# Optimization experiments

Hardware: AMD Instinct MI355X
Metric: run time of the kernel (lower is better)

The kernel has to match this reference:

```python
import jax, jax.numpy as jnp
import numpy as np
import math

HEAD_DIM = 128
N_HEADS = 32
N_KV_HEADS = 8
HIDDEN = 4096
ROPE_BASE = 10000.0


def _rope_cos_sin(position_ids):
    # inv_freq: [D/2]
    inv_freq = 1.0 / (ROPE_BASE ** (jnp.arange(0, HEAD_DIM, 2, dtype=jnp.float32) / HEAD_DIM))
    freqs = position_ids.astype(jnp.float32)[..., None] * inv_freq  # [B,S,D/2]
    emb = jnp.concatenate([freqs, freqs], axis=-1)  # [B,S,D]
    return jnp.cos(emb), jnp.sin(emb)


def _rotate_half(x):
    x1, x2 = jnp.split(x, 2, axis=-1)
    return jnp.concatenate([-x2, x1], axis=-1)


def setup_inputs() -> dict:
    key = jax.random.key(0)
    ks = jax.random.split(key, 5)
    B, S = 1, 2048
    inp = {
        "hidden_states": jax.random.normal(ks[0], (B, S, HIDDEN), dtype=jnp.float32),
        "position_ids": jnp.arange(B * S, dtype=jnp.int32).reshape(B, S),
        "Wq": jax.random.normal(ks[1], (HIDDEN, N_HEADS * HEAD_DIM), dtype=jnp.float32) * 0.02,
        "Wk": jax.random.normal(ks[2], (HIDDEN, N_KV_HEADS * HEAD_DIM), dtype=jnp.float32) * 0.02,
        "Wv": jax.random.normal(ks[3], (HIDDEN, N_KV_HEADS * HEAD_DIM), dtype=jnp.float32) * 0.02,
        "Wo": jax.random.normal(ks[4], (N_HEADS * HEAD_DIM, HIDDEN), dtype=jnp.float32) * 0.02,
    }
    return inp


def reference(hidden_states, position_ids, Wq, Wk, Wv, Wo):
    B, S, _ = hidden_states.shape
    G = N_HEADS // N_KV_HEADS

    q = (hidden_states @ Wq).reshape(B, S, N_HEADS, HEAD_DIM).transpose(0, 2, 1, 3)      # [B,H,S,D]
    k = (hidden_states @ Wk).reshape(B, S, N_KV_HEADS, HEAD_DIM).transpose(0, 2, 1, 3)   # [B,Hkv,S,D]
    v = (hidden_states @ Wv).reshape(B, S, N_KV_HEADS, HEAD_DIM).transpose(0, 2, 1, 3)

    cos, sin = _rope_cos_sin(position_ids)          # [B,S,D]
    cos = cos[:, None, :, :]                         # [B,1,S,D]
    sin = sin[:, None, :, :]
    q = q * cos + _rotate_half(q) * sin
    k = k * cos + _rotate_half(k) * sin

    # GQA head expansion (repeat_interleave over head dim)
    k = jnp.repeat(k, G, axis=1)                     # [B,H,S,D]
    v = jnp.repeat(v, G, axis=1)

    scale = 1.0 / math.sqrt(HEAD_DIM)
    scores = jnp.einsum("bhqd,bhkd->bhqk", q, k) * scale  # [B,H,S,S]
    causal = jnp.triu(jnp.full((S, S), -jnp.inf, dtype=scores.dtype), k=1)
    scores = scores + causal[None, None]
    probs = jax.nn.softmax(scores.astype(jnp.float32), axis=-1).astype(q.dtype)
    ctx = jnp.einsum("bhqk,bhkd->bhqd", probs, v)    # [B,H,S,D]
    ctx = ctx.transpose(0, 2, 1, 3).reshape(B, S, N_HEADS * HEAD_DIM)
    return ctx @ Wo
```

## Files before the change

kernel.cpp:

```cpp
#include <hip/hip_runtime.h>
#include <hip/hip_bf16.h>
#include <math.h>

#define SEQ 2048
#define NHEADS 32
#define NKVH 8
#define HD 128
#define HIDDEN 4096
#define NQKV 6144

typedef unsigned short u16;
typedef unsigned int u32;
typedef __attribute__((ext_vector_type(8))) __bf16 bf16x8;
typedef __attribute__((ext_vector_type(4))) float f32x4;
typedef __attribute__((ext_vector_type(4))) u16 u16x4;
typedef __attribute__((ext_vector_type(4))) u32 u32x4;

__device__ __forceinline__ u16 f2bf(float f) {
  u32 u = __builtin_bit_cast(u32, f);
  u32 r = (u + 0x7fffu + ((u >> 16) & 1u)) >> 16;
  return (u16)r;
}
__device__ __forceinline__ float bf2f(u16 h) {
  return __builtin_bit_cast(float, ((u32)h) << 16);
}
__device__ __forceinline__ void gload_lds16(const void* g, void* l) {
  __builtin_amdgcn_global_load_lds(
      (const __attribute__((address_space(1))) u32*)g,
      (__attribute__((address_space(3))) u32*)l, 16, 0, 0);
}

#define BAR __builtin_amdgcn_s_barrier()
#define PRIO1 __builtin_amdgcn_s_setprio(1)
#define PRIO0 __builtin_amdgcn_s_setprio(0)
#define VMW(n) asm volatile("s_waitcnt vmcnt(" #n ")" ::: "memory")

__global__ void __launch_bounds__(256) prep_all(
    const float* __restrict__ hs, u16* __restrict__ Xb,
    const float* __restrict__ Wq, u16* __restrict__ Wqt,
    const float* __restrict__ Wk, u16* __restrict__ Wkt,
    const float* __restrict__ Wv, u16* __restrict__ Wvt) {
  const int bid = blockIdx.x;
  if (bid < 8192) {
    const int i = (bid * 256 + threadIdx.x) * 4;
    const float4 v = *(const float4*)(hs + i);
    u16x4 o;
    o.x = f2bf(v.x); o.y = f2bf(v.y); o.z = f2bf(v.z); o.w = f2bf(v.w);
    *(u16x4*)(Xb + i) = o;
    return;
  }
  __shared__ float tile[64][65];
  const float* src; u16* dst; int C, lc, tb;
  const int b2 = bid - 8192;
  if (b2 < 4096) { src = Wq; dst = Wqt; C = 4096; lc = 6; tb = b2; }
  else if (b2 < 5120) { src = Wk; dst = Wkt; C = 1024; lc = 4; tb = b2 - 4096; }
  else { src = Wv; dst = Wvt; C = 1024; lc = 4; tb = b2 - 5120; }
  const int r0 = (tb >> lc) * 64, c0 = (tb & ((1 << lc) - 1)) * 64;
  const int tx = threadIdx.x & 63, ty = threadIdx.x >> 6;
#pragma unroll
  for (int j = 0; j < 16; ++j)
    tile[ty + j * 4][tx] = src[(size_t)(r0 + ty + j * 4) * C + c0 + tx];
  __syncthreads();
#pragma unroll
  for (int j = 0; j < 16; ++j)
    dst[(size_t)(c0 + ty + j * 4) * 4096 + r0 + tx] = f2bf(tile[tx][ty + j * 4]);
}

__global__ void __launch_bounds__(256) post_qkv(u16* __restrict__ qkv, u16* __restrict__ vtb,
                                                const int* __restrict__ pos,
                                                const float* __restrict__ Wsrc,
                                                u16* __restrict__ Wdst) {
  const int bid = blockIdx.x;
  if (bid < 20480) {
    int idx, hoff, sshift;
    float oscale;
    if (bid < 16384) {
      idx = bid * 256 + threadIdx.x;
      hoff = ((idx >> 6) & 31) * 128;
      sshift = 11;
      oscale = 0.08838834764831845f * 1.44269504088896340f;
    } else {
      idx = (bid - 16384) * 256 + threadIdx.x;
      hoff = 4096 + ((idx >> 6) & 7) * 128;
      sshift = 9;
      oscale = 1.0f;
    }
    const int j = idx & 63;
    const int s = idx >> sshift;
    if (s >= SEQ) return;
    const float p = (float)pos[s];
    const float invf = __expf((float)j * -0.14391156831212787f);
    const float ang = p * invf;
    const float c = cosf(ang), sn = sinf(ang);
    u16* bp = qkv + (size_t)s * NQKV + hoff + j;
    const float x1 = bf2f(bp[0]), x2 = bf2f(bp[64]);
    bp[0] = f2bf((x1 * c - x2 * sn) * oscale);
    bp[64] = f2bf((x2 * c + x1 * sn) * oscale);
    return;
  }
  if (bid < 22528) {
    __shared__ u16 tile[32][34];
    const int b2 = bid - 20480;
    const int c0 = (b2 & 31) * 32, r0 = (b2 >> 5) * 32;
    const int tx = threadIdx.x & 31, ty = threadIdx.x >> 5;
#pragma unroll
    for (int i = 0; i < 4; ++i)
      tile[ty + i * 8][tx] = qkv[(size_t)(r0 + ty + i * 8) * NQKV + 5120 + c0 + tx];
    __syncthreads();
#pragma unroll
    for (int i = 0; i < 4; ++i)
      vtb[(size_t)(c0 + ty + i * 8) * 2048 + r0 + tx] = tile[tx][ty + i * 8];
    return;
  }
  __shared__ float tf[64][65];
  const int tb = bid - 22528;
  const int r0 = (tb >> 6) * 64, c0 = (tb & 63) * 64;
  const int tx = threadIdx.x & 63, ty = threadIdx.x >> 6;
#pragma unroll
  for (int j = 0; j < 16; ++j)
    tf[ty + j * 4][tx] = Wsrc[(size_t)(r0 + ty + j * 4) * 4096 + c0 + tx];
  __syncthreads();
#pragma unroll
  for (int j = 0; j < 16; ++j)
    Wdst[(size_t)(c0 + ty + j * 4) * 4096 + r0 + tx] = f2bf(tf[tx][ty + j * 4]);
}

__global__ void __launch_bounds__(512) gemm_qkv(
    const u16* __restrict__ A, const u16* __restrict__ B, u16* __restrict__ C) {
  __shared__ u16 As[2][256 * 64];
  __shared__ u16 Bs[2][192 * 64];
  const int t = threadIdx.x;
  const int lane = t & 63, w = t >> 6;
  const int wr = w >> 2, wc = w & 3;
  const int l15 = lane & 15, l4 = lane >> 4;

  const int bid = blockIdx.x;
  const int xcd = bid & 7, ii = bid >> 3;
  const int byt = xcd, bxt = ii;
  const int row0 = byt * 256, col0 = bxt * 192;

  auto stageA_part = [&](int buf, int tile, int gfirst) {
#pragma unroll
    for (int gg = 0; gg < 2; ++gg) {
      const int g = gfirst + gg * 2;
      const int o = (g * 512 + t) * 16;
      const int ridx = o >> 7;
      const int slot = (o >> 4) & 7;
      gload_lds16(A + (size_t)(row0 + ridx) * 4096 + (tile << 6) + ((slot ^ (ridx & 7)) << 3),
                  (char*)&As[buf][0] + o);
    }
  };
  auto stageB = [&](int buf, int tile) {
#pragma unroll
    for (int g = 0; g < 3; ++g) {
      const int o = (g * 512 + t) * 16;
      const int ridx = o >> 7;
      const int slot = (o >> 4) & 7;
      gload_lds16(B + (size_t)(col0 + ridx) * 4096 + (tile << 6) + ((slot ^ (ridx & 7)) << 3),
                  (char*)&Bs[buf][0] + o);
    }
  };

  bf16x8 af[4][2], bfr[3][2];
  auto loadA = [&](int buf, int mh) {
#pragma unroll
    for (int f = 0; f < 4; ++f)
#pragma unroll
      for (int ks = 0; ks < 2; ++ks) {
        const int idx2 = wr * 128 + mh * 64 + f * 16 + l15;
        const int slot = ks * 4 + l4;
        af[f][ks] = *(const bf16x8*)((const char*)&As[buf][0] + idx2 * 128 +
                                     ((slot ^ (idx2 & 7)) << 4));
      }
  };
  auto loadB = [&](int buf) {
#pragma unroll
    for (int e = 0; e < 3; ++e)
#pragma unroll
      for (int ks = 0; ks < 2; ++ks) {
        const int idx2 = wc * 48 + e * 16 + l15;
        const int slot = ks * 4 + l4;
        bfr[e][ks] = *(const bf16x8*)((const char*)&Bs[buf][0] + idx2 * 128 +
                                      ((slot ^ (idx2 & 7)) << 4));
      }
  };

  f32x4 acc0[4][3], acc1[4][3];
#pragma unroll
  for (int f = 0; f < 4; ++f)
#pragma unroll
    for (int e = 0; e < 3; ++e) {
      acc0[f][e] = f32x4{0.f, 0.f, 0.f, 0.f};
      acc1[f][e] = f32x4{0.f, 0.f, 0.f, 0.f};
    }

  const int nkt = 4096 >> 6;

  stageA_part(0, 0, 0); stageA_part(0, 0, 1); stageB(0, 0);
  stageA_part(1, 1, 0); stageA_part(1, 1, 1); stageB(1, 1);
  VMW(7);
  BAR;

  for (int kt = 0; kt < nkt; ++kt) {
    const int buf = kt & 1;
    loadA(buf, 0); loadB(buf);
    if (kt >= 1 && kt + 1 < nkt) { stageA_part(buf ^ 1, kt + 1, 1); stageB(buf ^ 1, kt + 1); }
    BAR;
    PRIO1;
#pragma unroll
    for (int f = 0; f < 4; ++f)
#pragma unroll
      for (int e = 0; e < 3; ++e)
#pragma unroll
        for (int ks = 0; ks < 2; ++ks)
          acc0[f][e] = __builtin_amdgcn_mfma_f32_16x16x32_bf16(af[f][ks], bfr[e][ks], acc0[f][e],
                                                               0, 0, 0);
    PRIO0;
    BAR;
    loadA(buf, 1);
    if (kt + 2 < nkt) stageA_part(buf, kt + 2, 0);
    BAR;
    PRIO1;
#pragma unroll
    for (int f = 0; f < 4; ++f)
#pragma unroll
      for (int e = 0; e < 3; ++e)
#pragma unroll
        for (int ks = 0; ks < 2; ++ks)
          acc1[f][e] = __builtin_amdgcn_mfma_f32_16x16x32_bf16(af[f][ks], bfr[e][ks], acc1[f][e],
                                                               0, 0, 0);
    PRIO0;
    if (kt + 2 < nkt) { VMW(2); } else { VMW(0); }
    BAR;
  }

#pragma unroll
  for (int f = 0; f < 4; ++f)
#pragma unroll
    for (int e = 0; e < 3; ++e) {
      const int colb = col0 + wc * 48 + e * 16 + l15;
      const int r0a = row0 + wr * 128 + f * 16 + l4 * 4;
#pragma unroll
      for (int r = 0; r < 4; ++r)
        C[(size_t)(r0a + r) * NQKV + colb] = f2bf(acc0[f][e][r]);
      const int r0b = r0a + 64;
#pragma unroll
      for (int r = 0; r < 4; ++r)
        C[(size_t)(r0b + r) * NQKV + colb] = f2bf(acc1[f][e][r]);
    }
}

template <int MH, int NH>
__device__ __forceinline__ void mfq16(f32x4 (&acc)[4][4], const bf16x8 (&af)[2][2],
                                      const bf16x8 (&b)[2][2]) {
#pragma unroll
  for (int f = 0; f < 2; ++f)
#pragma unroll
    for (int e = 0; e < 2; ++e)
#pragma unroll
      for (int ks = 0; ks < 2; ++ks)
        acc[MH * 2 + f][NH * 2 + e] = __builtin_amdgcn_mfma_f32_16x16x32_bf16(
            af[f][ks], b[e][ks], acc[MH * 2 + f][NH * 2 + e], 0, 0, 0);
}

__global__ void __launch_bounds__(512, 2) gemm8p16(
    const u16* __restrict__ A, const u16* __restrict__ B, float* __restrict__ C) {
  __shared__ u16 As[2][2][64 * 64];
  __shared__ u16 Bs[2][2][128 * 64];
  const int t = threadIdx.x;
  const int lane = t & 63, w = t >> 6;
  const int wr = w >> 2, wc = w & 3;
  const int l15 = lane & 15, l4 = lane >> 4;

  const int flat = blockIdx.x;
  const int xcd = flat & 7, idx = flat >> 3;
  const int bxt = idx & 15, byt = xcd * 2 + (idx >> 4);
  const int row0 = byt * 128, col0 = bxt * 256;

  auto stageA = [&](int buf, int half, int tile) {
    const int o = t * 16;
    const int ridx = o >> 7;
    const int slot = (o >> 4) & 7;
    const int gr = (ridx >> 5) * 64 + half * 32 + (ridx & 31);
    gload_lds16(A + (size_t)(row0 + gr) * 4096 + (tile << 6) + ((slot ^ (ridx & 7)) << 3),
                (char*)&As[buf][half][0] + o);
  };
  auto stageB = [&](int buf, int half, int tile) {
#pragma unroll
    for (int g = 0; g < 2; ++g) {
      const int o = (g * 512 + t) * 16;
      const int ridx = o >> 7;
      const int slot = (o >> 4) & 7;
      const int gn = (ridx >> 5) * 64 + half * 32 + (ridx & 31);
      gload_lds16(B + (size_t)(col0 + gn) * 4096 + (tile << 6) + ((slot ^ (ridx & 7)) << 3),
                  (char*)&Bs[buf][half][0] + o);
    }
  };

  bf16x8 af[2][2], bf0[2][2], bf1[2][2];
  auto loadA = [&](int buf, int half) {
#pragma unroll
    for (int f = 0; f < 2; ++f)
#pragma unroll
      for (int ks = 0; ks < 2; ++ks) {
        const int idx2 = wr * 32 + f * 16 + l15;
        const int slot = ks * 4 + l4;
        af[f][ks] = *(const bf16x8*)((const char*)&As[buf][half][0] + idx2 * 128 +
                                     ((slot ^ (idx2 & 7)) << 4));
      }
  };
  auto loadB = [&](int buf, int half, bf16x8 (&dst)[2][2]) {
#pragma unroll
    for (int e = 0; e < 2; ++e)
#pragma unroll
      for (int ks = 0; ks < 2; ++ks) {
        const int idx2 = wc * 32 + e * 16 + l15;
        const int slot = ks * 4 + l4;
        dst[e][ks] = *(const bf16x8*)((const char*)&Bs[buf][half][0] + idx2 * 128 +
                                      ((slot ^ (idx2 & 7)) << 4));
      }
  };

  f32x4 acc[4][4];
#pragma unroll
  for (int m_ = 0; m_ < 4; ++m_)
#pragma unroll
    for (int n_ = 0; n_ < 4; ++n_) acc[m_][n_] = f32x4{0.f, 0.f, 0.f, 0.f};

  const int nit = (4096 >> 6) >> 1;

  stageA(0, 0, 0); stageB(0, 0, 0); stageB(0, 1, 0); stageA(0, 1, 0);
  stageA(1, 0, 1); stageB(1, 0, 1); stageB(1, 1, 1); stageA(1, 1, 1);
  VMW(6);
  BAR;

  for (int i = 0; i < nit; ++i) {
    const int tb = 2 * i;
    const bool g2 = (i + 1 < nit);
    loadA(0, 0); loadB(0, 0, bf0);
    BAR; PRIO1; mfq16<0, 0>(acc, af, bf0); PRIO0; BAR;
    loadB(0, 1, bf1);
    if (g2) { stageA(0, 0, tb + 2); stageB(0, 0, tb + 2); }
    BAR; PRIO1; mfq16<0, 1>(acc, af, bf1); PRIO0; BAR;
    loadA(0, 1);
    if (g2) stageB(0, 1, tb + 2);
    BAR; PRIO1; mfq16<1, 1>(acc, af, bf1); PRIO0; BAR;
    if (g2) stageA(0, 1, tb + 2);
    BAR; PRIO1; mfq16<1, 0>(acc, af, bf0); PRIO0;
    if (g2) { VMW(6); } else { VMW(0); }
    BAR;
    loadA(1, 0); loadB(1, 0, bf0);
    BAR; PRIO1; mfq16<0, 0>(acc, af, bf0); PRIO0; BAR;
    loadB(1, 1, bf1);
    if (g2) { stageA(1, 0, tb + 3); stageB(1, 0, tb + 3); }
    BAR; PRIO1; mfq16<0, 1>(acc, af, bf1); PRIO0; BAR;
    loadA(1, 1);
    if (g2) stageB(1, 1, tb + 3);
    BAR; PRIO1; mfq16<1, 1>(acc, af, bf1); PRIO0; BAR;
    if (g2) stageA(1, 1, tb + 3);
    BAR; PRIO1; mfq16<1, 0>(acc, af, bf0); PRIO0;
    if (g2) { VMW(6); }
    BAR;
  }

#pragma unroll
  for (int am = 0; am < 4; ++am) {
    const int rowb = row0 + wr * 64 + (am >> 1) * 32 + (am & 1) * 16 + l4 * 4;
#pragma unroll
    for (int an = 0; an < 4; ++an) {
      const int colb = col0 + wc * 64 + (an >> 1) * 32 + (an & 1) * 16 + l15;
#pragma unroll
      for (int r = 0; r < 4; ++r)
        C[(size_t)(rowb + r) * 4096 + colb] = acc[am][an][r];
    }
  }
}

__device__ __forceinline__ void stage_kv512(const u16* __restrict__ qkv, const u16* __restrict__ vt,
                                            const int kvh, const int kv0, u16* KsB, u16* VsB,
                                            const int t) {
#pragma unroll
  for (int i = 0; i < 2; ++i) {
    const int o = (i * 512 + t) * 16;
    const int row = o >> 8;
    const int slot = (o >> 4) & 15;
    gload_lds16(qkv + (size_t)(kv0 + row) * NQKV + 4096 + kvh * HD + ((slot ^ (row & 7)) << 3),
                (char*)KsB + o);
  }
#pragma unroll
  for (int i = 0; i < 2; ++i) {
    const int o = (i * 512 + t) * 16;
    const int row = o >> 7;
    const int slot = (o >> 4) & 7;
    gload_lds16(vt + (size_t)(kvh * HD + row) * SEQ + kv0 + ((slot ^ (row & 7)) << 3),
                (char*)VsB + o);
  }
}

__global__ void __launch_bounds__(512) attn_fwd(const u16* __restrict__ qkv,
                                                const u16* __restrict__ vt, u16* __restrict__ ctx) {
  __shared__ u16 Ks[2][64 * 128];
  __shared__ u16 Vs[2][128 * 64];
  const int t = threadIdx.x, lane = t & 63, w = t >> 6;
  const int bid = blockIdx.x;
  const int xcd = bid & 7, bi = bid >> 3;
  const int h = xcd * 4 + (bi & 3);
  const int j = bi >> 2;
  const int qbb = (j < 8) ? (15 - j) : (j - 8);
  const int kvh = xcd;
  const int q0 = qbb * 128;
  const int sq_base = q0 + w * 16;
  const int l15 = lane & 15, l4 = lane >> 4;
  const int sq_abs = sq_base + l15;
  const int bw = sq_base >> 6;

  bf16x8 qf[4];
  {
    const u16* qp = qkv + (size_t)sq_abs * NQKV + h * HD + l4 * 8;
#pragma unroll
    for (int kb = 0; kb < 4; ++kb) qf[kb] = *(const bf16x8*)(qp + kb * 32);
  }
  f32x4 po[8];
#pragma unroll
  for (int i = 0; i < 8; ++i) po[i] = f32x4{0.f, 0.f, 0.f, 0.f};
  float mrow = -1e30f;
  float lrow = 0.f;

  const int nb = 2 * qbb + 2;
  stage_kv512(qkv, vt, kvh, 0, Ks[0], Vs[0], t);
  __syncthreads();
  int cur = 0;

  for (int b = 0; b < nb; ++b) {
    if (b + 1 < nb) stage_kv512(qkv, vt, kvh, (b + 1) * 64, Ks[cur ^ 1], Vs[cur ^ 1], t);

    if (b <= bw) {
      f32x4 st[4];
#pragma unroll
      for (int c = 0; c < 4; ++c) st[c] = f32x4{0.f, 0.f, 0.f, 0.f};
#pragma unroll
      for (int c = 0; c < 4; ++c) {
        const int row = c * 16 + l15;
#pragma unroll
        for (int kb = 0; kb < 4; ++kb) {
          const int slot = kb * 4 + l4;
          bf16x8 bk = *(const bf16x8*)((const char*)Ks[cur] + row * 256 + ((slot ^ (row & 7)) << 4));
          st[c] = __builtin_amdgcn_mfma_f32_16x16x32_bf16(bk, qf[kb], st[c], 0, 0, 0);
        }
      }

      if (b == bw) {
#pragma unroll
        for (int c = 0; c < 4; ++c)
#pragma unroll
          for (int r = 0; r < 4; ++r) {
            const int sk = b * 64 + c * 16 + l4 * 4 + r;
            if (sk > sq_abs) st[c][r] = -1e30f;
          }
      }

      float rmax = -3e38f;
#pragma unroll
      for (int c = 0; c < 4; ++c)
        rmax = fmaxf(rmax, fmaxf(fmaxf(st[c][0], st[c][1]), fmaxf(st[c][2], st[c][3])));
      rmax = fmaxf(rmax, __shfl_xor(rmax, 16, 64));
      rmax = fmaxf(rmax, __shfl_xor(rmax, 32, 64));

      const bool skip = __all(rmax <= mrow + 8.f);
      const float mnew = skip ? mrow : fmaxf(mrow, rmax);

      float rs = 0.f;
#pragma unroll
      for (int c = 0; c < 4; ++c) {
        const float e0 = exp2f(st[c][0] - mnew), e1 = exp2f(st[c][1] - mnew);
        const float e2 = exp2f(st[c][2] - mnew), e3 = exp2f(st[c][3] - mnew);
        st[c][0] = e0; st[c][1] = e1; st[c][2] = e2; st[c][3] = e3;
        rs += (e0 + e1) + (e2 + e3);
      }
      rs += __shfl_xor(rs, 16, 64);
      rs += __shfl_xor(rs, 32, 64);

      if (!skip) {
        const float alpha = exp2f(mrow - mnew);
        mrow = mnew;
        lrow = lrow * alpha + rs;
        float av[4];
#pragma unroll
        for (int r = 0; r < 4; ++r) av[r] = __shfl(alpha, l4 * 4 + r, 16);
#pragma unroll
        for (int db = 0; db < 8; ++db)
#pragma unroll
          for (int r = 0; r < 4; ++r) po[db][r] *= av[r];
      } else {
        lrow += rs;
      }

      u32 pk[4][2];
#pragma unroll
      for (int c = 0; c < 4; ++c) {
        pk[c][0] = (u32)f2bf(st[c][0]) | ((u32)f2bf(st[c][1]) << 16);
        pk[c][1] = (u32)f2bf(st[c][2]) | ((u32)f2bf(st[c][3]) << 16);
      }
      const int src01 = l15 + ((lane & 16) << 1);
      const int src23 = src01 + 16;
      const bool lo = (lane & 32) == 0;
#pragma unroll
      for (int kb2 = 0; kb2 < 2; ++kb2) {
        const int c0 = kb2 * 2, c1 = c0 + 1;
        const u32 a0 = (u32)__shfl((int)pk[c0][0], src01, 64);
        const u32 a1 = (u32)__shfl((int)pk[c0][1], src01, 64);
        const u32 a2 = (u32)__shfl((int)pk[c0][0], src23, 64);
        const u32 a3 = (u32)__shfl((int)pk[c0][1], src23, 64);
        const u32 b0 = (u32)__shfl((int)pk[c1][0], src01, 64);
        const u32 b1 = (u32)__shfl((int)pk[c1][1], src01, 64);
        const u32 b2 = (u32)__shfl((int)pk[c1][0], src23, 64);
        const u32 b3 = (u32)__shfl((int)pk[c1][1], src23, 64);
        u32x4 wq;
        wq.x = lo ? a0 : b0;
        wq.y = lo ? a1 : b1;
        wq.z = lo ? a2 : b2;
        wq.w = lo ? a3 : b3;
        const bf16x8 pa = __builtin_bit_cast(bf16x8, wq);
#pragma unroll
        for (int db = 0; db < 8; ++db) {
          const int vrow = db * 16 + l15;
          const int pslot = kb2 * 4 + l4;
          bf16x8 bv =
              *(const bf16x8*)((const char*)Vs[cur] + vrow * 128 + ((pslot ^ (vrow & 7)) << 4));
          po[db] = __builtin_amdgcn_mfma_f32_16x16x32_bf16(pa, bv, po[db], 0, 0, 0);
        }
      }
    }
    __syncthreads();
    cur ^= 1;
  }

  float rl[4];
#pragma unroll
  for (int r = 0; r < 4; ++r) rl[r] = 1.f / __shfl(lrow, l4 * 4 + r, 16);
#pragma unroll
  for (int db = 0; db < 8; ++db)
#pragma unroll
    for (int r = 0; r < 4; ++r) {
      const int sq = sq_base + l4 * 4 + r;
      const int d = db * 16 + l15;
      ctx[(size_t)sq * (NHEADS * HD) + h * HD + d] = f2bf(po[db][r] * rl[r]);
    }
}

extern "C" void kernel_launch(void* const* d_in, const int* in_sizes, int n_in,
                              void* d_out, int out_size, void* d_ws, size_t ws_size,
                              hipStream_t stream) {
  const float* hs = (const float*)d_in[0];
  const int* pos = (const int*)d_in[1];
  const float* Wq = (const float*)d_in[2];
  const float* Wk = (const float*)d_in[3];
  const float* Wv = (const float*)d_in[4];
  const float* Wo = (const float*)d_in[5];

  u16* ws = (u16*)d_ws;
  u16* Xb = ws;
  u16* Wqt = Xb + (size_t)2048 * 4096;
  u16* Wkt = Wqt + (size_t)4096 * 4096;
  u16* Wvt = Wkt + (size_t)1024 * 4096;
  u16* Wot = Wvt + (size_t)1024 * 4096;
  u16* qkvb = Wot + (size_t)4096 * 4096;
  u16* vtb = qkvb + (size_t)2048 * 6144;
  u16* ctx = vtb + (size_t)1024 * 2048;
  const size_t need = ((size_t)(ctx - ws) + (size_t)2048 * 4096) * 2;
  if (ws_size < need) return;

  prep_all<<<14336, 256, 0, stream>>>(hs, Xb, Wq, Wqt, Wk, Wkt, Wv, Wvt);

  gemm_qkv<<<256, 512, 0, stream>>>(Xb, Wqt, qkvb);

  post_qkv<<<26624, 256, 0, stream>>>(qkvb, vtb, pos, Wo, Wot);

  attn_fwd<<<512, 512, 0, stream>>>(qkvb, vtb, ctx);

  gemm8p16<<<256, 512, 0, stream>>>(ctx, Wot, (float*)d_out);
}
```

Measured before the change: 317.1 us.

## Restructure output projection GEMM to 256x128 tiles with single-phase double buffering

Replaces the 128x256 ping-pong output GEMM with a 256x128 tile kernel in which each wave computes two 64-row halves against shared B fragments. Staging is simplified to one K-tile per buffer, with A loaded in parts interleaved across the two MFMA phases. Block-to-XCD mapping changes so each XCD owns one 256-row band. It drops the two-blocks-per-CU launch bound, which trades occupancy for more registers per wave, and the reworked pipeline may expose load latency.

```diff
diff --git a/kernel.cpp b/kernel.cpp
--- a/kernel.cpp
+++ b/kernel.cpp
@@ -250,130 +250,129 @@
     }
 }
 
-template <int MH, int NH>
-__device__ __forceinline__ void mfq16(f32x4 (&acc)[4][4], const bf16x8 (&af)[2][2],
-                                      const bf16x8 (&b)[2][2]) {
-#pragma unroll
-  for (int f = 0; f < 2; ++f)
-#pragma unroll
-    for (int e = 0; e < 2; ++e)
-#pragma unroll
-      for (int ks = 0; ks < 2; ++ks)
-        acc[MH * 2 + f][NH * 2 + e] = __builtin_amdgcn_mfma_f32_16x16x32_bf16(
-            af[f][ks], b[e][ks], acc[MH * 2 + f][NH * 2 + e], 0, 0, 0);
-}
-
-__global__ void __launch_bounds__(512, 2) gemm8p16(
+__global__ void __launch_bounds__(512) gemm_wo(
     const u16* __restrict__ A, const u16* __restrict__ B, float* __restrict__ C) {
-  __shared__ u16 As[2][2][64 * 64];
-  __shared__ u16 Bs[2][2][128 * 64];
+  __shared__ u16 As[2][256 * 64];
+  __shared__ u16 Bs[2][128 * 64];
   const int t = threadIdx.x;
   const int lane = t & 63, w = t >> 6;
   const int wr = w >> 2, wc = w & 3;
   const int l15 = lane & 15, l4 = lane >> 4;
 
-  const int flat = blockIdx.x;
-  const int xcd = flat & 7, idx = flat >> 3;
-  const int bxt = idx & 15, byt = xcd * 2 + (idx >> 4);
-  const int row0 = byt * 128, col0 = bxt * 256;
-
-  auto stageA = [&](int buf, int half, int tile) {
-    const int o = t * 16;
-    const int ridx = o >> 7;
-    const int slot = (o >> 4) & 7;
-    const int gr = (ridx >> 5) * 64 + half * 32 + (ridx & 31);
-    gload_lds16(A + (size_t)(row0 + gr) * 4096 + (tile << 6) + ((slot ^ (ridx & 7)) << 3),
-                (char*)&As[buf][half][0] + o);
-  };
-  auto stageB = [&](int buf, int half, int tile) {
+  const int bid = blockIdx.x;
+  const int xcd = bid & 7, ii = bid >> 3;
+  const int byt = xcd, bxt = ii;
+  const int row0 = byt * 256, col0 = bxt * 128;
+
+  auto stageA_part = [&](int buf, int tile, int gfirst) {
+#pragma unroll
+    for (int gg = 0; gg < 2; ++gg) {
+      const int g = gfirst + gg * 2;
+      const int o = (g * 512 + t) * 16;
+      const int ridx = o >> 7;
+      const int slot = (o >> 4) & 7;
+      gload_lds16(A + (size_t)(row0 + ridx) * 4096 + (tile << 6) + ((slot ^ (ridx & 7)) << 3),
+                  (char*)&As[buf][0] + o);
+    }
+  };
+  auto stageB = [&](int buf, int tile) {
 #pragma unroll
     for (int g = 0; g < 2; ++g) {
       const int o = (g * 512 + t) * 16;
       const int ridx = o >> 7;
       const int slot = (o >> 4) & 7;
-      const int gn = (ridx >> 5) * 64 + half * 32 + (ridx & 31);
-      gload_lds16(B + (size_t)(col0 + gn) * 4096 + (tile << 6) + ((slot ^ (ridx & 7)) << 3),
-                  (char*)&Bs[buf][half][0] + o);
-    }
-  };
-
-  bf16x8 af[2][2], bf0[2][2], bf1[2][2];
-  auto loadA = [&](int buf, int half) {
-#pragma unroll
-    for (int f = 0; f < 2; ++f)
+      gload_lds16(B + (size_t)(col0 + ridx) * 4096 + (tile << 6) + ((slot ^ (ridx & 7)) << 3),
+                  (char*)&Bs[buf][0] + o);
+    }
+  };
+
+  bf16x8 af[4][2], bfr[2][2];
+  auto loadA = [&](int buf, int mh) {
+#pragma unroll
+    for (int f = 0; f < 4; ++f)
 #pragma unroll
       for (int ks = 0; ks < 2; ++ks) {
-        const int idx2 = wr * 32 + f * 16 + l15;
+        const int idx2 = wr * 128 + mh * 64 + f * 16 + l15;
         const int slot = ks * 4 + l4;
-        af[f][ks] = *(const bf16x8*)((const char*)&As[buf][half][0] + idx2 * 128 +
+        af[f][ks] = *(const bf16x8*)((const char*)&As[buf][0] + idx2 * 128 +
                                      ((slot ^ (idx2 & 7)) << 4));
       }
   };
-  auto loadB = [&](int buf, int half, bf16x8 (&dst)[2][2]) {
+  auto loadB = [&](int buf) {
 #pragma unroll
     for (int e = 0; e < 2; ++e)
 #pragma unroll
       for (int ks = 0; ks < 2; ++ks) {
         const int idx2 = wc * 32 + e * 16 + l15;
         const int slot = ks * 4 + l4;
-        dst[e][ks] = *(const bf16x8*)((const char*)&Bs[buf][half][0] + idx2 * 128 +
+        bfr[e][ks] = *(const bf16x8*)((const char*)&Bs[buf][0] + idx2 * 128 +
                                       ((slot ^ (idx2 & 7)) << 4));
       }
   };
 
-  f32x4 acc[4][4];
-#pragma unroll
-  for (int m_ = 0; m_ < 4; ++m_)
-#pragma unroll
-    for (int n_ = 0; n_ < 4; ++n_) acc[m_][n_] = f32x4{0.f, 0.f, 0.f, 0.f};
-
-  const int nit = (4096 >> 6) >> 1;
-
-  stageA(0, 0, 0); stageB(0, 0, 0); stageB(0, 1, 0); stageA(0, 1, 0);
-  stageA(1, 0, 1); stageB(1, 0, 1); stageB(1, 1, 1); stageA(1, 1, 1);
+  f32x4 acc0[4][2], acc1[4][2];
+#pragma unroll
+  for (int f = 0; f < 4; ++f)
+#pragma unroll
+    for (int e = 0; e < 2; ++e) {
+      acc0[f][e] = f32x4{0.f, 0.f, 0.f, 0.f};
+      acc1[f][e] = f32x4{0.f, 0.f, 0.f, 0.f};
+    }
+
+  const int nkt = 4096 >> 6;
+
+  stageA_part(0, 0, 0); stageA_part(0, 0, 1); stageB(0, 0);
+  stageA_part(1, 1, 0); stageA_part(1, 1, 1); stageB(1, 1);
   VMW(6);
   BAR;
 
-  for (int i = 0; i < nit; ++i) {
-    const int tb = 2 * i;
-    const bool g2 = (i + 1 < nit);
-    loadA(0, 0); loadB(0, 0, bf0);
-    BAR; PRIO1; mfq16<0, 0>(acc, af, bf0); PRIO0; BAR;
-    loadB(0, 1, bf1);
-    if (g2) { stageA(0, 0, tb + 2); stageB(0, 0, tb + 2); }
-    BAR; PRIO1; mfq16<0, 1>(acc, af, bf1); PRIO0; BAR;
-    loadA(0, 1);
-    if (g2) stageB(0, 1, tb + 2);
-    BAR; PRIO1; mfq16<1, 1>(acc, af, bf1); PRIO0; BAR;
-    if (g2) stageA(0, 1, tb + 2);
-    BAR; PRIO1; mfq16<1, 0>(acc, af, bf0); PRIO0;
-    if (g2) { VMW(6); } else { VMW(0); }
-    BAR;
-    loadA(1, 0); loadB(1, 0, bf0);
-    BAR; PRIO1; mfq16<0, 0>(acc, af, bf0); PRIO0; BAR;
-    loadB(1, 1, bf1);
-    if (g2) { stageA(1, 0, tb + 3); stageB(1, 0, tb + 3); }
-    BAR; PRIO1; mfq16<0, 1>(acc, af, bf1); PRIO0; BAR;
-    loadA(1, 1);
-    if (g2) stageB(1, 1, tb + 3);
-    BAR; PRIO1; mfq16<1, 1>(acc, af, bf1); PRIO0; BAR;
-    if (g2) stageA(1, 1, tb + 3);
-    BAR; PRIO1; mfq16<1, 0>(acc, af, bf0); PRIO0;
-    if (g2) { VMW(6); }
-    BAR;
-  }
-
-#pragma unroll
-  for (int am = 0; am < 4; ++am) {
-    const int rowb = row0 + wr * 64 + (am >> 1) * 32 + (am & 1) * 16 + l4 * 4;
-#pragma unroll
-    for (int an = 0; an < 4; ++an) {
-      const int colb = col0 + wc * 64 + (an >> 1) * 32 + (an & 1) * 16 + l15;
+  for (int kt = 0; kt < nkt; ++kt) {
+    const int buf = kt & 1;
+    loadA(buf, 0); loadB(buf);
+    if (kt >= 1 && kt + 1 < nkt) { stageA_part(buf ^ 1, kt + 1, 1); stageB(buf ^ 1, kt + 1); }
+    BAR;
+    PRIO1;
+#pragma unroll
+    for (int f = 0; f < 4; ++f)
+#pragma unroll
+      for (int e = 0; e < 2; ++e)
+#pragma unroll
+        for (int ks = 0; ks < 2; ++ks)
+          acc0[f][e] = __builtin_amdgcn_mfma_f32_16x16x32_bf16(af[f][ks], bfr[e][ks], acc0[f][e],
+                                                               0, 0, 0);
+    PRIO0;
+    BAR;
+    loadA(buf, 1);
+    if (kt + 2 < nkt) stageA_part(buf, kt + 2, 0);
+    BAR;
+    PRIO1;
+#pragma unroll
+    for (int f = 0; f < 4; ++f)
+#pragma unroll
+      for (int e = 0; e < 2; ++e)
+#pragma unroll
+        for (int ks = 0; ks < 2; ++ks)
+          acc1[f][e] = __builtin_amdgcn_mfma_f32_16x16x32_bf16(af[f][ks], bfr[e][ks], acc1[f][e],
+                                                               0, 0, 0);
+    PRIO0;
+    if (kt + 2 < nkt) { VMW(2); } else { VMW(0); }
+    BAR;
+  }
+
+#pragma unroll
+  for (int f = 0; f < 4; ++f)
+#pragma unroll
+    for (int e = 0; e < 2; ++e) {
+      const int colb = col0 + wc * 32 + e * 16 + l15;
+      const int r0a = row0 + wr * 128 + f * 16 + l4 * 4;
 #pragma unroll
       for (int r = 0; r < 4; ++r)
-        C[(size_t)(rowb + r) * 4096 + colb] = acc[am][an][r];
-    }
-  }
+        C[(size_t)(r0a + r) * 4096 + colb] = acc0[f][e][r];
+      const int r0b = r0a + 64;
+#pragma unroll
+      for (int r = 0; r < 4; ++r)
+        C[(size_t)(r0b + r) * 4096 + colb] = acc1[f][e][r];
+    }
 }
 
 __device__ __forceinline__ void stage_kv512(const u16* __restrict__ qkv, const u16* __restrict__ vt,
@@ -578,5 +577,5 @@
 
   attn_fwd<<<512, 512, 0, stream>>>(qkvb, vtb, ctx);
 
-  gemm8p16<<<256, 512, 0, stream>>>(ctx, Wot, (float*)d_out);
-}
+  gemm_wo<<<256, 512, 0, stream>>>(ctx, Wot, (float*)d_out);
+}
```

Result: slower. 328.3 us (+3.5%).
